# Optimization experiments

Hardware: AMD Instinct MI355X
Metric: run time of the kernel (lower is better)

Reference implementation:

```python
import jax, jax.numpy as jnp
import numpy as np

B, Q, G = 32, 16384, 128   # batch, num queries, (padded) num GT per image
K = 32                      # first top-k (nearest candidates per GT)
N = 9                       # second top-k (highest-IoU matches per GT)


def box_cxcywh_to_xyxy(b):
    cx, cy, w, h = jnp.split(b, 4, axis=-1)
    return jnp.concatenate([cx - 0.5 * w, cy - 0.5 * h,
                            cx + 0.5 * w, cy + 0.5 * h], axis=-1)


def box_iou(a, b):
    # a, b: broadcastable [..., 4] in xyxy
    lt = jnp.maximum(a[..., :2], b[..., :2])
    rb = jnp.minimum(a[..., 2:], b[..., 2:])
    wh = jnp.clip(rb - lt, 0.0)
    inter = wh[..., 0] * wh[..., 1]
    area_a = (a[..., 2] - a[..., 0]) * (a[..., 3] - a[..., 1])
    area_b = (b[..., 2] - b[..., 0]) * (b[..., 3] - b[..., 1])
    return inter / (area_a + area_b - inter)


def _assign(gt, pred):
    # gt: [G,4] cxcywh, pred: [Q,4] cxcywh
    # euclidean cdist in cxcywh space: [G, Q]
    d = jnp.sqrt(jnp.sum((gt[:, None, :] - pred[None, :, :]) ** 2, axis=-1))
    # k nearest predictions per GT (smallest distance)
    _, kidx = jax.lax.top_k(-d, K)            # [G, K]
    k_boxes = pred[kidx]                       # [G, K, 4]
    iou = box_iou(box_cxcywh_to_xyxy(gt)[:, None, :],
                  box_cxcywh_to_xyxy(k_boxes))           # [G, K]
    vals, ns = jax.lax.top_k(iou, N)           # [G, N] highest IoU among the K
    pred_idx = jnp.take_along_axis(kidx, ns, axis=1)      # [G, N] global pred ids
    gt_idx = jnp.broadcast_to(jnp.arange(gt.shape[0])[:, None], ns.shape)
    return pred_idx.reshape(-1), gt_idx.reshape(-1)


def setup_inputs() -> dict:
    key = jax.random.key(0)
    k1, k2 = jax.random.split(key)
    pred_boxes = jax.random.uniform(k1, (B, Q, 4), dtype=jnp.float32)
    gt_boxes = jax.random.uniform(k2, (B, G, 4), dtype=jnp.float32)
    return {"pred_boxes": pred_boxes, "gt_boxes": gt_boxes}


def reference(pred_boxes, gt_boxes):
    # per-image assignment, vectorized over the batch
    pred_idx, gt_idx = jax.vmap(_assign)(gt_boxes, pred_boxes)
    # pred_idx, gt_idx: [B, G*N] int32 (analog of the list of (i, j) index tensors)
    return pred_idx, gt_idx
```

## Files before the change

### kernel.cpp

```cpp
#include <hip/hip_runtime.h>

#define BB 32
#define QQ 16384
#define GG 128
#define KK 32
#define NN 9
#define TT 16
#define TH 1024
#define RR (QQ / TH)
#define NW (TH / 64)
#define CAP 256
#define ACAP 128
#define UF 4

typedef unsigned long long u64;
typedef unsigned int u32;

#define INFF __uint_as_float(0x7F800000u)

__device__ __forceinline__ u64 pack_asc(float key, u32 idx) {
  return (((u64)__float_as_uint(key)) << 32) | (u64)idx;
}

__device__ __forceinline__ float dist2_ref(const float4 g, const float4 p) {
#pragma clang fp contract(off)
  float dx = g.x - p.x;
  float dy = g.y - p.y;
  float dz = g.z - p.z;
  float dw = g.w - p.w;
  float s = dx * dx + dy * dy;
  s = s + dz * dz;
  s = s + dw * dw;
  return s;
}

__device__ __forceinline__ float iou_ref(const float4 g, const float4 p) {
#pragma clang fp contract(off)
  float gx1 = g.x - 0.5f * g.z, gy1 = g.y - 0.5f * g.w;
  float gx2 = g.x + 0.5f * g.z, gy2 = g.y + 0.5f * g.w;
  float px1 = p.x - 0.5f * p.z, py1 = p.y - 0.5f * p.w;
  float px2 = p.x + 0.5f * p.z, py2 = p.y + 0.5f * p.w;
  float ltx = fmaxf(gx1, px1), lty = fmaxf(gy1, py1);
  float rbx = fminf(gx2, px2), rby = fminf(gy2, py2);
  float wx = fmaxf(rbx - ltx, 0.0f), wy = fmaxf(rby - lty, 0.0f);
  float inter = wx * wy;
  float aa = (gx2 - gx1) * (gy2 - gy1);
  float ab = (px2 - px1) * (py2 - py1);
  return inter / ((aa + ab) - inter);
}

__device__ __forceinline__ u64 bitonic64(u64 v, int lane) {
#pragma unroll
  for (int k = 2; k <= 64; k <<= 1) {
#pragma unroll
    for (int j = k >> 1; j > 0; j >>= 1) {
      u64 o = __shfl_xor(v, j, 64);
      bool up = ((lane & k) == 0);
      bool lower = ((lane & j) == 0);
      v = (lower == up) ? (v < o ? v : o) : (v > o ? v : o);
    }
  }
  return v;
}

__device__ __forceinline__ float bitonic64f(float v, int lane) {
#pragma unroll
  for (int k = 2; k <= 64; k <<= 1) {
#pragma unroll
    for (int j = k >> 1; j > 0; j >>= 1) {
      float o = __shfl_xor(v, j, 64);
      bool up = ((lane & k) == 0);
      bool lower = ((lane & j) == 0);
      v = (lower == up) ? fminf(v, o) : fmaxf(v, o);
    }
  }
  return v;
}

__global__ __launch_bounds__(TH, 4) void atss_kernel(
    const float4* __restrict__ pred, const float4* __restrict__ gtb,
    int* __restrict__ out) {
  __shared__ float smin[TT][TH];
  __shared__ float ckey[TT][CAP];
  __shared__ unsigned short cidx[TT][CAP];
  __shared__ unsigned short sact[TT][ACAP];
  __shared__ int kidx[TT][KK];
  __shared__ int nC[TT];
  __shared__ int nAct[TT];

  const int t = threadIdx.x;
  const int f = blockIdx.x;
  const int b = (f & 7) | ((f >> 6) << 3);
  const int g0 = ((f >> 3) & 7) * TT;

  if (t < TT) {
    nC[t] = 0;
    nAct[t] = 0;
  }

  float4 G[TT];
#pragma unroll
  for (int gg = 0; gg < TT; ++gg) G[gg] = gtb[b * GG + g0 + gg];

  const float4* pb = pred + (size_t)b * QQ;

  float mn[TT];
#pragma unroll
  for (int gg = 0; gg < TT; ++gg) mn[gg] = INFF;

  float4 P[UF];
#pragma unroll
  for (int u = 0; u < UF; ++u) P[u] = pb[t + u * TH];
#pragma unroll
  for (int j = 0; j < RR; j += UF) {
    float4 C[UF];
#pragma unroll
    for (int u = 0; u < UF; ++u) C[u] = P[u];
    if (j + UF < RR) {
#pragma unroll
      for (int u = 0; u < UF; ++u) P[u] = pb[t + (j + UF + u) * TH];
    }
#pragma unroll
    for (int u = 0; u < UF; ++u) {
      float4 p = C[u];
      float pp = fmaf(p.x, p.x, fmaf(p.y, p.y, fmaf(p.z, p.z, p.w * p.w)));
#pragma unroll
      for (int gg = 0; gg < TT; ++gg) {
        float dot = fmaf(G[gg].x, p.x,
                    fmaf(G[gg].y, p.y,
                    fmaf(G[gg].z, p.z, G[gg].w * p.w)));
        mn[gg] = fminf(mn[gg], fmaf(-2.0f, dot, pp));
      }
    }
  }
#pragma unroll
  for (int gg = 0; gg < TT; ++gg) smin[gg][t] = mn[gg];

  __syncthreads();

  const int w = t >> 6;
  const int lane = t & 63;

  const float4 gt = gtb[b * GG + g0 + w];

  float a = INFF;
#pragma unroll
  for (int k = 0; k < NW; ++k) a = fminf(a, smin[w][lane + k * 64]);
  float srt = bitonic64f(a, lane);
  float Us = __shfl(srt, 31, 64);
  float gg2 = fmaf(gt.x, gt.x,
              fmaf(gt.y, gt.y, fmaf(gt.z, gt.z, gt.w * gt.w)));
  const float sUs = Us + fabsf(Us) * 2e-5f + 4e-6f;
  const float T = fmaxf(Us + gg2, 0.0f) * 1.00002f + 4e-6f;

#pragma unroll
  for (int k = 0; k < NW; ++k) {
    int r = lane + k * 64;
    if (smin[w][r] <= sUs) {
      int pos = atomicAdd(&nAct[w], 1);
      if (pos < ACAP) sact[w][pos] = (unsigned short)r;
    }
  }
  int na = nAct[w];

  if (na <= ACAP) {
    for (int it = lane; it < na; it += 64) {
      int r = sact[w][it];
      for (int j = 0; j < RR; ++j) {
        int i = r + j * TH;
        float d2 = dist2_ref(gt, pb[i]);
        if (d2 <= T) {
          int pos = atomicAdd(&nC[w], 1);
          if (pos < CAP) {
            ckey[w][pos] = d2;
            cidx[w][pos] = (unsigned short)i;
          }
        }
      }
    }
  } else {
    for (int r = lane; r < TH; r += 64) {
      for (int j = 0; j < RR; ++j) {
        int i = r + j * TH;
        float d2 = dist2_ref(gt, pb[i]);
        if (d2 <= T) {
          int pos = atomicAdd(&nC[w], 1);
          if (pos < CAP) {
            ckey[w][pos] = d2;
            cidx[w][pos] = (unsigned short)i;
          }
        }
      }
    }
  }
  int n = nC[w];

  if (n > CAP) {
    if (lane == 0) {
      u64 best[KK];
      for (int l = 0; l < KK; ++l) best[l] = ~0ull;
      for (int i = 0; i < QQ; ++i) {
        float d = sqrtf(dist2_ref(gt, pb[i]));
        u64 pk = pack_asc(d, (u32)i);
        if (pk < best[KK - 1]) {
          int pos = KK - 1;
          while (pos > 0 && best[pos - 1] > pk) {
            best[pos] = best[pos - 1];
            --pos;
          }
          best[pos] = pk;
        }
      }
      for (int l = 0; l < KK; ++l) kidx[w][l] = (int)(best[l] & 0xFFFFFFFFull);
    }
  } else if (n <= 64) {
    u64 v = (lane < n) ? pack_asc(sqrtf(ckey[w][lane]), (u32)cidx[w][lane])
                       : ~0ull;
    u64 s = bitonic64(v, lane);
    if (lane < KK) kidx[w][lane] = (int)(s & 0xFFFFFFFFull);
  } else {
    volatile float* vk = ckey[w];
    for (int sel = 0; sel < KK; ++sel) {
      u64 lm = ~0ull;
      int ls = -1;
      for (int s = lane; s < n; s += 64) {
        float d = sqrtf(vk[s]);
        u64 pk = pack_asc(d, (u32)cidx[w][s]);
        if (pk < lm) {
          lm = pk;
          ls = s;
        }
      }
      u64 ww = lm;
#pragma unroll
      for (int j = 32; j > 0; j >>= 1) {
        u64 o = __shfl_xor(ww, j, 64);
        ww = o < ww ? o : ww;
      }
      if (lm == ww && ls >= 0) {
        vk[ls] = INFF;
        kidx[w][sel] = (int)(ww & 0xFFFFFFFFull);
      }
    }
  }

  {
    u64 v = ~0ull;
    if (lane < KK) {
      float iou = iou_ref(gt, pb[kidx[w][lane]]);
      v = (((u64)(~__float_as_uint(iou))) << 32) | (u64)lane;
    }
    u64 s = bitonic64(v, lane);
    if (lane < NN) {
      int pos = (int)(s & 0xFFFFFFFFull);
      int base = (b * GG + g0 + w) * NN + lane;
      out[base] = kidx[w][pos];
      out[BB * GG * NN + base] = g0 + w;
    }
  }
}

extern "C" void kernel_launch(void* const* d_in, const int* in_sizes, int n_in,
                              void* d_out, int out_size, void* d_ws, size_t ws_size,
                              hipStream_t stream) {
  (void)in_sizes;
  (void)n_in;
  (void)out_size;
  (void)d_ws;
  (void)ws_size;
  const float4* pred = (const float4*)d_in[0];
  const float4* gt = (const float4*)d_in[1];
  int* out = (int*)d_out;
  atss_kernel<<<(GG / TT) * BB, TH, 0, stream>>>(pred, gt, out);
}
```

Before: 95.45 us.

## Split fused kernel into min-pass and per-GT tail kernels via workspace

The single fused kernel becomes two launches. The first computes per-thread partial minimum distances for 8 GTs per block and writes them to a global workspace (16 MB). The second runs 512-thread blocks, one wavefront per GT, and does the threshold, candidate collection and top-k stages. The aim is more blocks with smaller GT tiles so the irregular tail and the main loop get better occupancy. The cost is an extra launch and a global round trip for the partial minima. The old fused kernel is kept as a fallback when the workspace is too small.

Result: faster. 91.38 us (-4.3%).

```diff
diff --git a/kernel.cpp b/kernel.cpp
--- a/kernel.cpp
+++ b/kernel.cpp
@@ -5,13 +5,16 @@
 #define GG 128
 #define KK 32
 #define NN 9
-#define TT 16
-#define TH 1024
-#define RR (QQ / TH)
-#define NW (TH / 64)
-#define CAP 256
-#define ACAP 128
+
+#define TTA 8
+#define THA 1024
+#define RRA (QQ / THA)
 #define UF 4
+
+#define THB 512
+#define NWB (THB / 64)
+#define CAPB 192
+#define ACAPB 64
 
 typedef unsigned long long u64;
 typedef unsigned int u32;
@@ -77,55 +80,46 @@
   return v;
 }
 
-__global__ __launch_bounds__(TH, 4) void atss_kernel(
+__device__ __forceinline__ void swz(int f, int& b, int& g0) {
+  b = (f & 7) * 4 + (f >> 7);
+  g0 = ((f >> 3) & 15) * TTA;
+}
+
+__global__ __launch_bounds__(THA, 4) void pass1_kernel(
     const float4* __restrict__ pred, const float4* __restrict__ gtb,
-    int* __restrict__ out) {
-  __shared__ float smin[TT][TH];
-  __shared__ float ckey[TT][CAP];
-  __shared__ unsigned short cidx[TT][CAP];
-  __shared__ unsigned short sact[TT][ACAP];
-  __shared__ int kidx[TT][KK];
-  __shared__ int nC[TT];
-  __shared__ int nAct[TT];
-
+    float* __restrict__ gsmin) {
   const int t = threadIdx.x;
-  const int f = blockIdx.x;
-  const int b = (f & 7) | ((f >> 6) << 3);
-  const int g0 = ((f >> 3) & 7) * TT;
-
-  if (t < TT) {
-    nC[t] = 0;
-    nAct[t] = 0;
-  }
-
-  float4 G[TT];
-#pragma unroll
-  for (int gg = 0; gg < TT; ++gg) G[gg] = gtb[b * GG + g0 + gg];
+  int b, g0;
+  swz(blockIdx.x, b, g0);
+
+  float4 G[TTA];
+#pragma unroll
+  for (int gg = 0; gg < TTA; ++gg) G[gg] = gtb[b * GG + g0 + gg];
 
   const float4* pb = pred + (size_t)b * QQ;
 
-  float mn[TT];
-#pragma unroll
-  for (int gg = 0; gg < TT; ++gg) mn[gg] = INFF;
+  float mn[TTA];
+#pragma unroll
+  for (int gg = 0; gg < TTA; ++gg) mn[gg] = INFF;
 
   float4 P[UF];
 #pragma unroll
-  for (int u = 0; u < UF; ++u) P[u] = pb[t + u * TH];
-#pragma unroll
-  for (int j = 0; j < RR; j += UF) {
+  for (int u = 0; u < UF; ++u) P[u] = pb[t + u * THA];
+#pragma unroll
+  for (int j = 0; j < RRA; j += UF) {
     float4 C[UF];
 #pragma unroll
     for (int u = 0; u < UF; ++u) C[u] = P[u];
-    if (j + UF < RR) {
-#pragma unroll
-      for (int u = 0; u < UF; ++u) P[u] = pb[t + (j + UF + u) * TH];
+    if (j + UF < RRA) {
+#pragma unroll
+      for (int u = 0; u < UF; ++u) P[u] = pb[t + (j + UF + u) * THA];
     }
 #pragma unroll
     for (int u = 0; u < UF; ++u) {
       float4 p = C[u];
       float pp = fmaf(p.x, p.x, fmaf(p.y, p.y, fmaf(p.z, p.z, p.w * p.w)));
 #pragma unroll
-      for (int gg = 0; gg < TT; ++gg) {
+      for (int gg = 0; gg < TTA; ++gg) {
         float dot = fmaf(G[gg].x, p.x,
                     fmaf(G[gg].y, p.y,
                     fmaf(G[gg].z, p.z, G[gg].w * p.w)));
@@ -134,18 +128,45 @@
     }
   }
 #pragma unroll
-  for (int gg = 0; gg < TT; ++gg) smin[gg][t] = mn[gg];
-
-  __syncthreads();
-
+  for (int gg = 0; gg < TTA; ++gg)
+    gsmin[(size_t)(b * GG + g0 + gg) * THA + t] = mn[gg];
+}
+
+__global__ __launch_bounds__(THB, 4) void tail_kernel(
+    const float4* __restrict__ pred, const float4* __restrict__ gtb,
+    const float* __restrict__ gsmin, int* __restrict__ out) {
+  __shared__ float ckey[NWB][CAPB];
+  __shared__ unsigned short cidx[NWB][CAPB];
+  __shared__ unsigned short sact[NWB][ACAPB];
+  __shared__ int kidx[NWB][KK];
+  __shared__ int nC[NWB];
+  __shared__ int nAct[NWB];
+
+  const int t = threadIdx.x;
   const int w = t >> 6;
   const int lane = t & 63;
-
-  const float4 gt = gtb[b * GG + g0 + w];
-
+  int b, g0;
+  swz(blockIdx.x, b, g0);
+  const int g = g0 + w;
+  const int task = b * GG + g;
+
+  if (lane == 0) {
+    nC[w] = 0;
+    nAct[w] = 0;
+  }
+
+  const float4 gt = gtb[task];
+  const float4* pb = pred + (size_t)b * QQ;
+  const float* sm = gsmin + (size_t)task * THA;
+
+  float4 V[4];
+#pragma unroll
+  for (int m = 0; m < 4; ++m) V[m] = ((const float4*)sm)[lane * 4 + m];
   float a = INFF;
 #pragma unroll
-  for (int k = 0; k < NW; ++k) a = fminf(a, smin[w][lane + k * 64]);
+  for (int m = 0; m < 4; ++m)
+    a = fminf(a, fminf(fminf(V[m].x, V[m].y), fminf(V[m].z, V[m].w)));
+
   float srt = bitonic64f(a, lane);
   float Us = __shfl(srt, 31, 64);
   float gg2 = fmaf(gt.x, gt.x,
@@ -154,24 +175,27 @@
   const float T = fmaxf(Us + gg2, 0.0f) * 1.00002f + 4e-6f;
 
 #pragma unroll
-  for (int k = 0; k < NW; ++k) {
-    int r = lane + k * 64;
-    if (smin[w][r] <= sUs) {
-      int pos = atomicAdd(&nAct[w], 1);
-      if (pos < ACAP) sact[w][pos] = (unsigned short)r;
+  for (int m = 0; m < 4; ++m) {
+    float vv[4] = {V[m].x, V[m].y, V[m].z, V[m].w};
+#pragma unroll
+    for (int q = 0; q < 4; ++q) {
+      if (vv[q] <= sUs) {
+        int pos = atomicAdd(&nAct[w], 1);
+        if (pos < ACAPB) sact[w][pos] = (unsigned short)(lane * 16 + m * 4 + q);
+      }
     }
   }
   int na = nAct[w];
 
-  if (na <= ACAP) {
+  if (na <= ACAPB) {
     for (int it = lane; it < na; it += 64) {
       int r = sact[w][it];
-      for (int j = 0; j < RR; ++j) {
-        int i = r + j * TH;
+      for (int j = 0; j < RRA; ++j) {
+        int i = r + j * THA;
         float d2 = dist2_ref(gt, pb[i]);
         if (d2 <= T) {
           int pos = atomicAdd(&nC[w], 1);
-          if (pos < CAP) {
+          if (pos < CAPB) {
             ckey[w][pos] = d2;
             cidx[w][pos] = (unsigned short)i;
           }
@@ -179,13 +203,13 @@
       }
     }
   } else {
-    for (int r = lane; r < TH; r += 64) {
-      for (int j = 0; j < RR; ++j) {
-        int i = r + j * TH;
+    for (int r = lane; r < THA; r += 64) {
+      for (int j = 0; j < RRA; ++j) {
+        int i = r + j * THA;
         float d2 = dist2_ref(gt, pb[i]);
         if (d2 <= T) {
           int pos = atomicAdd(&nC[w], 1);
-          if (pos < CAP) {
+          if (pos < CAPB) {
             ckey[w][pos] = d2;
             cidx[w][pos] = (unsigned short)i;
           }
@@ -195,7 +219,7 @@
   }
   int n = nC[w];
 
-  if (n > CAP) {
+  if (n > CAPB) {
     if (lane == 0) {
       u64 best[KK];
       for (int l = 0; l < KK; ++l) best[l] = ~0ull;
@@ -253,6 +277,193 @@
     u64 s = bitonic64(v, lane);
     if (lane < NN) {
       int pos = (int)(s & 0xFFFFFFFFull);
+      int base = task * NN + lane;
+      out[base] = kidx[w][pos];
+      out[BB * GG * NN + base] = g;
+    }
+  }
+}
+
+#define TTF 16
+#define THF 1024
+#define RRF (QQ / THF)
+#define NWF (THF / 64)
+#define CAPF 256
+#define ACAPF 128
+
+__global__ __launch_bounds__(THF, 4) void atss_fused(
+    const float4* __restrict__ pred, const float4* __restrict__ gtb,
+    int* __restrict__ out) {
+  __shared__ float smin[TTF][THF];
+  __shared__ float ckey[TTF][CAPF];
+  __shared__ unsigned short cidx[TTF][CAPF];
+  __shared__ unsigned short sact[TTF][ACAPF];
+  __shared__ int kidx[TTF][KK];
+  __shared__ int nC[TTF];
+  __shared__ int nAct[TTF];
+
+  const int t = threadIdx.x;
+  const int f = blockIdx.x;
+  const int b = (f & 7) | ((f >> 6) << 3);
+  const int g0 = ((f >> 3) & 7) * TTF;
+
+  if (t < TTF) {
+    nC[t] = 0;
+    nAct[t] = 0;
+  }
+
+  float4 G[TTF];
+#pragma unroll
+  for (int gg = 0; gg < TTF; ++gg) G[gg] = gtb[b * GG + g0 + gg];
+  const float4* pb = pred + (size_t)b * QQ;
+
+  float mn[TTF];
+#pragma unroll
+  for (int gg = 0; gg < TTF; ++gg) mn[gg] = INFF;
+  float4 P[UF];
+#pragma unroll
+  for (int u = 0; u < UF; ++u) P[u] = pb[t + u * THF];
+#pragma unroll
+  for (int j = 0; j < RRF; j += UF) {
+    float4 C[UF];
+#pragma unroll
+    for (int u = 0; u < UF; ++u) C[u] = P[u];
+    if (j + UF < RRF) {
+#pragma unroll
+      for (int u = 0; u < UF; ++u) P[u] = pb[t + (j + UF + u) * THF];
+    }
+#pragma unroll
+    for (int u = 0; u < UF; ++u) {
+      float4 p = C[u];
+      float pp = fmaf(p.x, p.x, fmaf(p.y, p.y, fmaf(p.z, p.z, p.w * p.w)));
+#pragma unroll
+      for (int gg = 0; gg < TTF; ++gg) {
+        float dot = fmaf(G[gg].x, p.x,
+                    fmaf(G[gg].y, p.y,
+                    fmaf(G[gg].z, p.z, G[gg].w * p.w)));
+        mn[gg] = fminf(mn[gg], fmaf(-2.0f, dot, pp));
+      }
+    }
+  }
+#pragma unroll
+  for (int gg = 0; gg < TTF; ++gg) smin[gg][t] = mn[gg];
+
+  __syncthreads();
+
+  const int w = t >> 6;
+  const int lane = t & 63;
+  const float4 gt = gtb[b * GG + g0 + w];
+
+  float a = INFF;
+#pragma unroll
+  for (int k = 0; k < NWF; ++k) a = fminf(a, smin[w][lane + k * 64]);
+  float srt = bitonic64f(a, lane);
+  float Us = __shfl(srt, 31, 64);
+  float gg2 = fmaf(gt.x, gt.x,
+              fmaf(gt.y, gt.y, fmaf(gt.z, gt.z, gt.w * gt.w)));
+  const float sUs = Us + fabsf(Us) * 2e-5f + 4e-6f;
+  const float T = fmaxf(Us + gg2, 0.0f) * 1.00002f + 4e-6f;
+
+#pragma unroll
+  for (int k = 0; k < NWF; ++k) {
+    int r = lane + k * 64;
+    if (smin[w][r] <= sUs) {
+      int pos = atomicAdd(&nAct[w], 1);
+      if (pos < ACAPF) sact[w][pos] = (unsigned short)r;
+    }
+  }
+  int na = nAct[w];
+
+  if (na <= ACAPF) {
+    for (int it = lane; it < na; it += 64) {
+      int r = sact[w][it];
+      for (int j = 0; j < RRF; ++j) {
+        int i = r + j * THF;
+        float d2 = dist2_ref(gt, pb[i]);
+        if (d2 <= T) {
+          int pos = atomicAdd(&nC[w], 1);
+          if (pos < CAPF) {
+            ckey[w][pos] = d2;
+            cidx[w][pos] = (unsigned short)i;
+          }
+        }
+      }
+    }
+  } else {
+    for (int r = lane; r < THF; r += 64) {
+      for (int j = 0; j < RRF; ++j) {
+        int i = r + j * THF;
+        float d2 = dist2_ref(gt, pb[i]);
+        if (d2 <= T) {
+          int pos = atomicAdd(&nC[w], 1);
+          if (pos < CAPF) {
+            ckey[w][pos] = d2;
+            cidx[w][pos] = (unsigned short)i;
+          }
+        }
+      }
+    }
+  }
+  int n = nC[w];
+
+  if (n > CAPF) {
+    if (lane == 0) {
+      u64 best[KK];
+      for (int l = 0; l < KK; ++l) best[l] = ~0ull;
+      for (int i = 0; i < QQ; ++i) {
+        float d = sqrtf(dist2_ref(gt, pb[i]));
+        u64 pk = pack_asc(d, (u32)i);
+        if (pk < best[KK - 1]) {
+          int pos = KK - 1;
+          while (pos > 0 && best[pos - 1] > pk) {
+            best[pos] = best[pos - 1];
+            --pos;
+          }
+          best[pos] = pk;
+        }
+      }
+      for (int l = 0; l < KK; ++l) kidx[w][l] = (int)(best[l] & 0xFFFFFFFFull);
+    }
+  } else if (n <= 64) {
+    u64 v = (lane < n) ? pack_asc(sqrtf(ckey[w][lane]), (u32)cidx[w][lane])
+                       : ~0ull;
+    u64 s = bitonic64(v, lane);
+    if (lane < KK) kidx[w][lane] = (int)(s & 0xFFFFFFFFull);
+  } else {
+    volatile float* vk = ckey[w];
+    for (int sel = 0; sel < KK; ++sel) {
+      u64 lm = ~0ull;
+      int ls = -1;
+      for (int s = lane; s < n; s += 64) {
+        float d = sqrtf(vk[s]);
+        u64 pk = pack_asc(d, (u32)cidx[w][s]);
+        if (pk < lm) {
+          lm = pk;
+          ls = s;
+        }
+      }
+      u64 ww = lm;
+#pragma unroll
+      for (int j = 32; j > 0; j >>= 1) {
+        u64 o = __shfl_xor(ww, j, 64);
+        ww = o < ww ? o : ww;
+      }
+      if (lm == ww && ls >= 0) {
+        vk[ls] = INFF;
+        kidx[w][sel] = (int)(ww & 0xFFFFFFFFull);
+      }
+    }
+  }
+
+  {
+    u64 v = ~0ull;
+    if (lane < KK) {
+      float iou = iou_ref(gt, pb[kidx[w][lane]]);
+      v = (((u64)(~__float_as_uint(iou))) << 32) | (u64)lane;
+    }
+    u64 s = bitonic64(v, lane);
+    if (lane < NN) {
+      int pos = (int)(s & 0xFFFFFFFFull);
       int base = (b * GG + g0 + w) * NN + lane;
       out[base] = kidx[w][pos];
       out[BB * GG * NN + base] = g0 + w;
@@ -266,10 +477,16 @@
   (void)in_sizes;
   (void)n_in;
   (void)out_size;
-  (void)d_ws;
-  (void)ws_size;
   const float4* pred = (const float4*)d_in[0];
   const float4* gt = (const float4*)d_in[1];
   int* out = (int*)d_out;
-  atss_kernel<<<(GG / TT) * BB, TH, 0, stream>>>(pred, gt, out);
-}
+
+  const size_t need = (size_t)BB * GG * THA * sizeof(float);
+  if (ws_size >= need) {
+    float* gsmin = (float*)d_ws;
+    pass1_kernel<<<(GG / TTA) * BB, THA, 0, stream>>>(pred, gt, gsmin);
+    tail_kernel<<<(GG / TTA) * BB, THB, 0, stream>>>(pred, gt, gsmin, out);
+  } else {
+    atss_fused<<<(GG / TTF) * BB, THF, 0, stream>>>(pred, gt, out);
+  }
+}
```

## Halve GTs per block, tighten threshold with top-2 residue minima

Applied to the files above, without the earlier changes.

Each block now handles 8 GT boxes instead of 16, which doubles the grid and lowers per-thread register pressure (launch bounds raised to 8). Only 8 of the 16 waves do the selection phase; the rest exit early. The candidate threshold is now the 32nd smallest of the per-residue top-2 minima, merged via two bitonic sorts and a bitonic merge. This is a tighter bound than the 32nd smallest per-residue minimum, so fewer residues become active and fewer loads are rescanned. In exchange the prediction array is read twice as many times overall in the first pass, and half the threads sit idle in the second phase.

Result: faster. 79.04 us (median of 2 runs) (-17.2%).

```diff
diff --git a/kernel.cpp b/kernel.cpp
--- a/kernel.cpp
+++ b/kernel.cpp
@@ -5,12 +5,12 @@
 #define GG 128
 #define KK 32
 #define NN 9
-#define TT 16
+#define TT 8
 #define TH 1024
 #define RR (QQ / TH)
 #define NW (TH / 64)
-#define CAP 256
-#define ACAP 128
+#define CAP 192
+#define ACAP 96
 #define UF 4
 
 typedef unsigned long long u64;
@@ -77,7 +77,7 @@
   return v;
 }
 
-__global__ __launch_bounds__(TH, 4) void atss_kernel(
+__global__ __launch_bounds__(TH, 8) void atss_kernel(
     const float4* __restrict__ pred, const float4* __restrict__ gtb,
     int* __restrict__ out) {
   __shared__ float smin[TT][TH];
@@ -90,8 +90,8 @@
 
   const int t = threadIdx.x;
   const int f = blockIdx.x;
-  const int b = (f & 7) | ((f >> 6) << 3);
-  const int g0 = ((f >> 3) & 7) * TT;
+  const int b = (f & 7) * 4 + (f >> 7);
+  const int g0 = ((f >> 3) & 15) * TT;
 
   if (t < TT) {
     nC[t] = 0;
@@ -140,14 +140,33 @@
 
   const int w = t >> 6;
   const int lane = t & 63;
+  if (w >= TT) return;
 
   const float4 gt = gtb[b * GG + g0 + w];
 
-  float a = INFF;
-#pragma unroll
-  for (int k = 0; k < NW; ++k) a = fminf(a, smin[w][lane + k * 64]);
-  float srt = bitonic64f(a, lane);
-  float Us = __shfl(srt, 31, 64);
+  float V[NW];
+#pragma unroll
+  for (int k = 0; k < NW; ++k) V[k] = smin[w][lane + 64 * k];
+
+  float m1 = INFF, m2 = INFF;
+#pragma unroll
+  for (int k = 0; k < NW; ++k) {
+    float v = V[k];
+    float nm1 = fminf(m1, v);
+    m2 = fminf(m2, fmaxf(m1, v));
+    m1 = nm1;
+  }
+
+  float A = bitonic64f(m1, lane);
+  float Bs = bitonic64f(m2, lane);
+  float Br = __shfl(Bs, 63 - lane, 64);
+  float m = fminf(A, Br);
+#pragma unroll
+  for (int j = 32; j > 0; j >>= 1) {
+    float o = __shfl_xor(m, j, 64);
+    m = ((lane & j) == 0) ? fminf(m, o) : fmaxf(m, o);
+  }
+  float Us = __shfl(m, 31, 64);
   float gg2 = fmaf(gt.x, gt.x,
               fmaf(gt.y, gt.y, fmaf(gt.z, gt.z, gt.w * gt.w)));
   const float sUs = Us + fabsf(Us) * 2e-5f + 4e-6f;
@@ -155,10 +174,9 @@
 
 #pragma unroll
   for (int k = 0; k < NW; ++k) {
-    int r = lane + k * 64;
-    if (smin[w][r] <= sUs) {
+    if (V[k] <= sUs) {
       int pos = atomicAdd(&nAct[w], 1);
-      if (pos < ACAP) sact[w][pos] = (unsigned short)r;
+      if (pos < ACAP) sact[w][pos] = (unsigned short)(lane + 64 * k);
     }
   }
   int na = nAct[w];
```
